# Optimization experiments

Hardware: AMD Instinct MI355X
Metric: run time of the kernel (lower is better)

Reference implementation:

```python
import jax, jax.numpy as jnp
import numpy as np

N_HEADS = 16
D_HEAD = 64
N_ROTATE = 32
ROPE_BASE = 10000.0
MAX_LEN = 2048  # round_up_to_multiple_of_256(keep count); static for jit
BATCH, SEQ = 2, 4096


def setup_inputs() -> dict:
    key = jax.random.key(0)
    kq, kk, kv = jax.random.split(key, 3)
    q = jax.random.normal(kq, (BATCH, N_HEADS, MAX_LEN, D_HEAD), jnp.float32)
    k = jax.random.normal(kk, (BATCH, N_HEADS, SEQ, D_HEAD), jnp.float32)
    v = jax.random.normal(kv, (BATCH, N_HEADS, SEQ, D_HEAD), jnp.float32)
    # causal full mask [batch, seq, seq] and full position ids [batch, seq]
    mask_full = jnp.broadcast_to(jnp.tril(jnp.ones((SEQ, SEQ), bool)), (BATCH, SEQ, SEQ))
    pos_full = jnp.broadcast_to(jnp.arange(SEQ, dtype=jnp.int32), (BATCH, SEQ))
    # skip_mask: exactly MAX_LEN kept tokens per row (random positions)
    rng = np.random.default_rng(0)
    sm = np.zeros((BATCH, SEQ), dtype=bool)
    for i in range(BATCH):
        sm[i, rng.permutation(SEQ)[:MAX_LEN]] = True
    return {"q": q, "k": k, "v": v, "mask_full": mask_full,
            "pos_full": pos_full, "skip_mask": jnp.asarray(sm)}


def _rope_rotate(x, pos):
    # x: [b, h, L, n_rotate], pos: [b, L]
    half = N_ROTATE // 2
    inv_freq = 1.0 / (ROPE_BASE ** (jnp.arange(0, N_ROTATE, 2, dtype=jnp.float32) / N_ROTATE))
    freqs = pos.astype(jnp.float32)[..., None] * inv_freq          # [b, L, half]
    emb = jnp.concatenate([freqs, freqs], axis=-1)[:, None]        # [b, 1, L, n_rotate]
    cos, sin = jnp.cos(emb), jnp.sin(emb)
    x1, x2 = x[..., :half], x[..., half:]
    rot = jnp.concatenate([-x2, x1], axis=-1)                      # rotate_half
    return x * cos + rot * sin


def reference(q, k, v, mask_full, pos_full, skip_mask):
    b, S = skip_mask.shape
    lengths = skip_mask.sum(axis=1)
    # vectorized _trim_attention_mask: stable argsort compacts kept indices to the front
    order = jnp.argsort(jnp.where(skip_mask, 0, 1), axis=1, stable=True)
    idx = order[:, :MAX_LEN]                                       # [b, max_len]
    brow = jnp.arange(b)[:, None]
    mask_trim = mask_full[brow, idx]                               # [b, max_len, S]
    pos_trim = pos_full[brow, idx]                                 # [b, max_len]
    valid = jnp.arange(MAX_LEN)[None, :] < lengths[:, None]
    mask_trim = mask_trim & valid[..., None]
    pos_trim = jnp.where(valid, pos_trim, 0)

    # partial RoPE on first n_rotate channels
    rq = _rope_rotate(q[..., :N_ROTATE], pos_trim)
    rk = _rope_rotate(k[..., :N_ROTATE], pos_full)
    q = jnp.concatenate([rq, q[..., N_ROTATE:]], axis=-1)
    k = jnp.concatenate([rk, k[..., N_ROTATE:]], axis=-1)

    # masked SDPA (bool mask broadcast over heads)
    scale = 1.0 / jnp.sqrt(jnp.float32(D_HEAD))
    scores = jnp.einsum('bhqd,bhkd->bhqk', q, k) * scale
    scores = jnp.where(mask_trim[:, None], scores, jnp.finfo(scores.dtype).min)
    attn = jax.nn.softmax(scores, axis=-1)
    return jnp.einsum('bhqk,bhkd->bhqd', attn, v)
```

## Files before the change

### kernel.cpp

```cpp
#include <hip/hip_runtime.h>
#include <math.h>

#define BB 2
#define HH 16
#define QQ 2048
#define SS 4096
#define DD 64
#define NRH 16
#define NQT 32
#define PBPAD 68

typedef unsigned short u16;
typedef unsigned int   u32;
typedef short bhalf8 __attribute__((ext_vector_type(8)));
typedef float f32x4  __attribute__((ext_vector_type(4)));

typedef __attribute__((address_space(1))) const u32 gu32;
typedef __attribute__((address_space(3))) u32 lu32;

#if __has_builtin(__builtin_amdgcn_exp2f)
#define EXP2(x) __builtin_amdgcn_exp2f(x)
#else
#define EXP2(x) exp2f(x)
#endif

union Frag16 { uint4 u; bhalf8 v; u16 s[8]; uint2 d[2]; };

__device__ __forceinline__ u16 f2bf(float f) {
  union { float f; u32 u; } c; c.f = f;
  return (u16)((c.u + 0x7FFFu + ((c.u >> 16) & 1u)) >> 16);
}

__device__ __forceinline__ bhalf8 ldfrag(const u16* p) {
  Frag16 f; f.u = *reinterpret_cast<const uint4*>(p); return f.v;
}

__device__ __forceinline__ void rope32(float* x, int pos) {
  const float step = 0.8304820237218405f;
  const float fp = (float)pos;
#pragma unroll
  for (int i = 0; i < NRH; ++i) {
    float ang = fp * exp2f(-step * (float)i);
    float sv, cv;
    __sincosf(ang, &sv, &cv);
    float a = x[i], b = x[i + NRH];
    x[i]       = a * cv - b * sv;
    x[i + NRH] = b * cv + a * sv;
  }
}

__global__ void prep_idx_kernel(const unsigned char* __restrict__ sm,
                                int* __restrict__ idx) {
  __shared__ int wsum[4];
  __shared__ int modes;
  const int tid = threadIdx.x;
  const int b = (int)blockIdx.x;

  int c = 0;
  for (int i = 0; i < 32; ++i) c += (sm[tid * 32 + i] != 0) ? 1 : 0;
#pragma unroll
  for (int off = 32; off; off >>= 1) c += __shfl_down(c, off);
  if ((tid & 63) == 0) wsum[tid >> 6] = c;
  __syncthreads();
  if (tid == 0) modes = (wsum[0] + wsum[1] + wsum[2] + wsum[3] > 3000) ? 1 : 0;
  __syncthreads();
  const bool byteMode = (modes != 0);
  const u32* sm32 = (const u32*)sm;

  const int base = b * SS + tid * 16;
  u32 flags = 0;
  for (int i = 0; i < 16; ++i) {
    bool f = byteMode ? (sm[base + i] != 0) : (sm32[base + i] != 0);
    flags |= ((u32)(f ? 1 : 0)) << i;
  }
  int cnt = __popc(flags);
  int vv = cnt;
#pragma unroll
  for (int off = 1; off < 64; off <<= 1) {
    int t = __shfl_up(vv, off);
    if ((tid & 63) >= off) vv += t;
  }
  __syncthreads();
  if ((tid & 63) == 63) wsum[tid >> 6] = vv;
  __syncthreads();
  int add = 0;
  for (int w2 = 0; w2 < (tid >> 6); ++w2) add += wsum[w2];
  int p = vv - cnt + add;
  for (int i = 0; i < 16; ++i) {
    if (flags & (1u << i)) {
      if (p < QQ) idx[b * QQ + p] = tid * 16 + i;
      ++p;
    }
  }
}

__global__ __launch_bounds__(256) void prep_kv_kernel(const float* __restrict__ k,
                                                      const float* __restrict__ v,
                                                      u16* __restrict__ kbf,
                                                      u16* __restrict__ vt) {
  __shared__ u16 tile[64][72];
  if (blockIdx.x < 512) {
    int r = blockIdx.x * 256 + threadIdx.x;
    int pos = r & (SS - 1);
    float x[64];
    const float4* src = (const float4*)(k + (size_t)r * DD);
#pragma unroll
    for (int i = 0; i < 16; ++i) {
      float4 t = src[i];
      x[4 * i] = t.x; x[4 * i + 1] = t.y; x[4 * i + 2] = t.z; x[4 * i + 3] = t.w;
    }
    rope32(x, pos);
    u16 tmp[64];
#pragma unroll
    for (int i = 0; i < 64; ++i) tmp[i] = f2bf(x[i]);
    uint4* dst = (uint4*)(kbf + (size_t)r * DD);
#pragma unroll
    for (int i = 0; i < 8; ++i) dst[i] = ((uint4*)tmp)[i];
  } else {
    int blk = (int)blockIdx.x - 512;
    int bh = blk >> 6;
    int jt = blk & 63;
    int t = threadIdx.x;
    int jl = t >> 2;
    int dc = (t & 3) * 16;
    const float4* src = (const float4*)(v + ((size_t)(bh * SS + jt * 64 + jl)) * DD + dc);
#pragma unroll
    for (int i = 0; i < 4; ++i) {
      float4 f = src[i];
      tile[jl][dc + 4 * i]     = f2bf(f.x);
      tile[jl][dc + 4 * i + 1] = f2bf(f.y);
      tile[jl][dc + 4 * i + 2] = f2bf(f.z);
      tile[jl][dc + 4 * i + 3] = f2bf(f.w);
    }
    __syncthreads();
    int d = t >> 2;
    int js = (t & 3) * 16;
    u16 o[16];
#pragma unroll
    for (int i = 0; i < 16; ++i) o[i] = tile[js + i][d];
    uint4* dst = (uint4*)(vt + ((size_t)(bh * DD + d)) * SS + jt * 64 + js);
    dst[0] = ((uint4*)o)[0];
    dst[1] = ((uint4*)o)[1];
  }
}

__device__ __forceinline__ void stage_tiles(const char* kb_bh, const char* vt_bh,
                                            u16* Kb, u16* Vb, int t0,
                                            int w, int srow, int schk) {
#pragma unroll
  for (int p2 = 0; p2 < 2; ++p2) {
    const int rr = w * 16 + p2 * 8 + srow;
    {
      const char* g = kb_bh + (size_t)(t0 + rr) * 128 + ((schk ^ (rr & 7)) * 16);
      lu32* l = (lu32*)((char*)Kb + (w * 16 + p2 * 8) * 128);
      __builtin_amdgcn_global_load_lds((gu32*)g, l, 16, 0, 0);
    }
    {
      const char* g = vt_bh + (size_t)rr * (SS * 2) + t0 * 2 + ((schk ^ (rr & 7)) * 16);
      lu32* l = (lu32*)((char*)Vb + (w * 16 + p2 * 8) * 128);
      __builtin_amdgcn_global_load_lds((gu32*)g, l, 16, 0, 0);
    }
  }
}

__device__ __forceinline__ void attn_tile(
    const u16* __restrict__ Kb, const u16* __restrict__ Vb, u16* __restrict__ pb,
    int t0, int grp, int col,
    int bnd0, int bnd1, int bnd2, int bnd3,
    bhalf8 qa0, bhalf8 qa1,
    f32x4& acc0, f32x4& acc1, f32x4& acc2, f32x4& acc3,
    float& l0, float& l1, float& l2, float& l3) {
  const int swz = col & 7;
  f32x4 s0 = {0.f, 0.f, 0.f, 0.f}, s1 = s0, s2 = s0, s3 = s0;
  {
    const u16* kr0 = Kb + (0 * 16 + col) * 64;
    const u16* kr1 = Kb + (1 * 16 + col) * 64;
    const u16* kr2 = Kb + (2 * 16 + col) * 64;
    const u16* kr3 = Kb + (3 * 16 + col) * 64;
    s0 = __builtin_amdgcn_mfma_f32_16x16x32_bf16(qa0, ldfrag(kr0 + ((grp ^ swz) * 8)), s0, 0, 0, 0);
    s1 = __builtin_amdgcn_mfma_f32_16x16x32_bf16(qa0, ldfrag(kr1 + ((grp ^ swz) * 8)), s1, 0, 0, 0);
    s2 = __builtin_amdgcn_mfma_f32_16x16x32_bf16(qa0, ldfrag(kr2 + ((grp ^ swz) * 8)), s2, 0, 0, 0);
    s3 = __builtin_amdgcn_mfma_f32_16x16x32_bf16(qa0, ldfrag(kr3 + ((grp ^ swz) * 8)), s3, 0, 0, 0);
    s0 = __builtin_amdgcn_mfma_f32_16x16x32_bf16(qa1, ldfrag(kr0 + (((4 + grp) ^ swz) * 8)), s0, 0, 0, 0);
    s1 = __builtin_amdgcn_mfma_f32_16x16x32_bf16(qa1, ldfrag(kr1 + (((4 + grp) ^ swz) * 8)), s1, 0, 0, 0);
    s2 = __builtin_amdgcn_mfma_f32_16x16x32_bf16(qa1, ldfrag(kr2 + (((4 + grp) ^ swz) * 8)), s2, 0, 0, 0);
    s3 = __builtin_amdgcn_mfma_f32_16x16x32_bf16(qa1, ldfrag(kr3 + (((4 + grp) ^ swz) * 8)), s3, 0, 0, 0);
  }

  const int key0 = t0 + col, key1 = t0 + 16 + col, key2 = t0 + 32 + col, key3 = t0 + 48 + col;
#define SM_ROW(R, BND, LACC)                                                   \
  {                                                                            \
    float p0 = (key0 <= (BND)) ? EXP2(s0[R] - 16.f) : 0.f;                     \
    float p1 = (key1 <= (BND)) ? EXP2(s1[R] - 16.f) : 0.f;                     \
    float p2v = (key2 <= (BND)) ? EXP2(s2[R] - 16.f) : 0.f;                    \
    float p3 = (key3 <= (BND)) ? EXP2(s3[R] - 16.f) : 0.f;                     \
    (LACC) += (p0 + p1) + (p2v + p3);                                          \
    u16* prow = pb + (grp * 4 + (R)) * PBPAD;                                  \
    prow[col] = f2bf(p0); prow[16 + col] = f2bf(p1);                           \
    prow[32 + col] = f2bf(p2v); prow[48 + col] = f2bf(p3);                     \
  }
  SM_ROW(0, bnd0, l0)
  SM_ROW(1, bnd1, l1)
  SM_ROW(2, bnd2, l2)
  SM_ROW(3, bnd3, l3)
#undef SM_ROW

  bhalf8 pa0, pa1;
  {
    const u16* p = pb + col * PBPAD;
    Frag16 f0, f1;
    f0.d[0] = *(const uint2*)(p + grp * 8);
    f0.d[1] = *(const uint2*)(p + grp * 8 + 4);
    f1.d[0] = *(const uint2*)(p + 32 + grp * 8);
    f1.d[1] = *(const uint2*)(p + 32 + grp * 8 + 4);
    pa0 = f0.v; pa1 = f1.v;
  }

  {
    const u16* vr0 = Vb + (0 * 16 + col) * 64;
    const u16* vr1 = Vb + (1 * 16 + col) * 64;
    const u16* vr2 = Vb + (2 * 16 + col) * 64;
    const u16* vr3 = Vb + (3 * 16 + col) * 64;
    acc0 = __builtin_amdgcn_mfma_f32_16x16x32_bf16(pa0, ldfrag(vr0 + ((grp ^ swz) * 8)), acc0, 0, 0, 0);
    acc1 = __builtin_amdgcn_mfma_f32_16x16x32_bf16(pa0, ldfrag(vr1 + ((grp ^ swz) * 8)), acc1, 0, 0, 0);
    acc2 = __builtin_amdgcn_mfma_f32_16x16x32_bf16(pa0, ldfrag(vr2 + ((grp ^ swz) * 8)), acc2, 0, 0, 0);
    acc3 = __builtin_amdgcn_mfma_f32_16x16x32_bf16(pa0, ldfrag(vr3 + ((grp ^ swz) * 8)), acc3, 0, 0, 0);
    acc0 = __builtin_amdgcn_mfma_f32_16x16x32_bf16(pa1, ldfrag(vr0 + (((4 + grp) ^ swz) * 8)), acc0, 0, 0, 0);
    acc1 = __builtin_amdgcn_mfma_f32_16x16x32_bf16(pa1, ldfrag(vr1 + (((4 + grp) ^ swz) * 8)), acc1, 0, 0, 0);
    acc2 = __builtin_amdgcn_mfma_f32_16x16x32_bf16(pa1, ldfrag(vr2 + (((4 + grp) ^ swz) * 8)), acc2, 0, 0, 0);
    acc3 = __builtin_amdgcn_mfma_f32_16x16x32_bf16(pa1, ldfrag(vr3 + (((4 + grp) ^ swz) * 8)), acc3, 0, 0, 0);
  }
}

__global__ __launch_bounds__(256) void attn_mfma_kernel(
    const float* __restrict__ qsrc, const u16* __restrict__ kbf,
    const u16* __restrict__ vt, const int* __restrict__ idx,
    float* __restrict__ out) {
  __shared__ u16 KbufA[64 * 64];
  __shared__ u16 VbufA[64 * 64];
  __shared__ u16 KbufB[64 * 64];
  __shared__ u16 VbufB[64 * 64];
  __shared__ u16 Pbuf[4][16 * PBPAD];

  const int blk = (int)blockIdx.x;
  const int bh  = blk & 31;
  const int pr  = blk >> 5;
  const int b   = bh >> 4;
  const int tid  = threadIdx.x;
  const int w    = tid >> 6;
  const int lane = tid & 63;
  const int grp  = lane >> 4;
  const int col  = lane & 15;

  const char* kb_bh = (const char*)(kbf + (size_t)bh * SS * DD);
  const char* vt_bh = (const char*)(vt + (size_t)bh * DD * SS);

  const int srow = lane >> 3;
  const int schk = lane & 7;

  u16* pb = Pbuf[w];

  for (int pass = 0; pass < 2; ++pass) {
    const int qt = pass ? (NQT - 1 - pr) : pr;
    const int q0 = qt * 64;

    const int bnd0 = idx[b * QQ + q0 + w * 16 + grp * 4 + 0];
    const int bnd1 = idx[b * QQ + q0 + w * 16 + grp * 4 + 1];
    const int bnd2 = idx[b * QQ + q0 + w * 16 + grp * 4 + 2];
    const int bnd3 = idx[b * QQ + q0 + w * 16 + grp * 4 + 3];
    const int maxbound = idx[b * QQ + q0 + 63];
    const int ntiles = (maxbound >> 6) + 1;

    bhalf8 qa0, qa1;
    {
      const int qrow = q0 + w * 16 + col;
      const int mypos = idx[b * QQ + qrow];
      const float* qr = qsrc + (size_t)(bh * QQ + qrow) * DD;
      const int lof = (grp & 1) * 8;
      float4 A0 = *(const float4*)(qr + lof);
      float4 A1 = *(const float4*)(qr + lof + 4);
      float4 B0 = *(const float4*)(qr + 16 + lof);
      float4 B1 = *(const float4*)(qr + 16 + lof + 4);
      float4 C0 = *(const float4*)(qr + 32 + grp * 8);
      float4 C1 = *(const float4*)(qr + 32 + grp * 8 + 4);
      float xlo[8] = {A0.x, A0.y, A0.z, A0.w, A1.x, A1.y, A1.z, A1.w};
      float xhi[8] = {B0.x, B0.y, B0.z, B0.w, B1.x, B1.y, B1.z, B1.w};
      float xq1[8] = {C0.x, C0.y, C0.z, C0.w, C1.x, C1.y, C1.z, C1.w};
      const float scq = 0.125f * 1.44269504088896f;
      const float fp = (float)mypos;
      Frag16 f0, f1;
#pragma unroll
      for (int j = 0; j < 8; ++j) {
        float ang = fp * exp2f(-0.8304820237218405f * (float)(lof + j));
        float sv, cv;
        __sincosf(ang, &sv, &cv);
        float val = (grp >= 2) ? (xhi[j] * cv + xlo[j] * sv)
                               : (xlo[j] * cv - xhi[j] * sv);
        f0.s[j] = f2bf(val * scq);
        f1.s[j] = f2bf(xq1[j] * scq);
      }
      qa0 = f0.v; qa1 = f1.v;
    }

    f32x4 acc0 = {0.f, 0.f, 0.f, 0.f}, acc1 = acc0, acc2 = acc0, acc3 = acc0;
    float l0 = 0.f, l1 = 0.f, l2 = 0.f, l3 = 0.f;

    stage_tiles(kb_bh, vt_bh, KbufA, VbufA, 0, w, srow, schk);
    __syncthreads();

    for (int ti = 0; ti < ntiles; ti += 2) {
      const bool has1 = (ti + 1) < ntiles;
      if (has1) stage_tiles(kb_bh, vt_bh, KbufB, VbufB, (ti + 1) << 6, w, srow, schk);
      attn_tile(KbufA, VbufA, pb, ti << 6, grp, col, bnd0, bnd1, bnd2, bnd3,
                qa0, qa1, acc0, acc1, acc2, acc3, l0, l1, l2, l3);
      __syncthreads();
      if (has1) {
        if (ti + 2 < ntiles)
          stage_tiles(kb_bh, vt_bh, KbufA, VbufA, (ti + 2) << 6, w, srow, schk);
        attn_tile(KbufB, VbufB, pb, (ti + 1) << 6, grp, col, bnd0, bnd1, bnd2, bnd3,
                  qa0, qa1, acc0, acc1, acc2, acc3, l0, l1, l2, l3);
        __syncthreads();
      }
    }

#pragma unroll
    for (int mdel = 1; mdel < 16; mdel <<= 1) {
      l0 += __shfl_xor(l0, mdel);
      l1 += __shfl_xor(l1, mdel);
      l2 += __shfl_xor(l2, mdel);
      l3 += __shfl_xor(l3, mdel);
    }
    float i0 = 1.f / l0, i1 = 1.f / l1, i2 = 1.f / l2, i3 = 1.f / l3;
    float* ob = out + (size_t)(bh * QQ + q0 + w * 16 + grp * 4) * DD + col;
#pragma unroll
    for (int r = 0; r < 4; ++r) {
      float iv = (r == 0) ? i0 : (r == 1) ? i1 : (r == 2) ? i2 : i3;
      ob[(size_t)r * DD + 0]  = acc0[r] * iv;
      ob[(size_t)r * DD + 16] = acc1[r] * iv;
      ob[(size_t)r * DD + 32] = acc2[r] * iv;
      ob[(size_t)r * DD + 48] = acc3[r] * iv;
    }
  }
}

__global__ __launch_bounds__(64) void attn_fb_kernel(const float* __restrict__ q,
                                                     const float* __restrict__ ksrc,
                                                     const float* __restrict__ v,
                                                     const int* __restrict__ idx,
                                                     float* __restrict__ out) {
  int t = (int)(gridDim.x - 1u - blockIdx.x);
  int sub = t >> 5;
  int bh = t & 31;
  int b = bh >> 4;
  int lane = threadIdx.x;
  int qi = sub * 64 + lane;
  const int bound = idx[b * QQ + qi];

  float qreg[64];
  {
    const float4* qp = (const float4*)(q + ((size_t)bh * QQ + qi) * DD);
#pragma unroll
    for (int i = 0; i < 16; ++i) {
      float4 t4 = qp[i];
      qreg[4 * i] = t4.x; qreg[4 * i + 1] = t4.y;
      qreg[4 * i + 2] = t4.z; qreg[4 * i + 3] = t4.w;
    }
  }
  rope32(qreg, bound);
#pragma unroll
  for (int i = 0; i < 64; ++i) qreg[i] *= 0.125f;

  const float* kbase = ksrc + (size_t)bh * SS * DD;
  const float* vbase = v + (size_t)bh * SS * DD;
  float acc[64];
#pragma unroll
  for (int i = 0; i < 64; ++i) acc[i] = 0.f;
  float mrun = -INFINITY, lrun = 0.f;

  for (int j = 0; j <= bound; ++j) {
    float ka[64];
    const float4* kp = (const float4*)(kbase + (size_t)j * DD);
#pragma unroll
    for (int i = 0; i < 16; ++i) {
      float4 t4 = kp[i];
      ka[4 * i] = t4.x; ka[4 * i + 1] = t4.y;
      ka[4 * i + 2] = t4.z; ka[4 * i + 3] = t4.w;
    }
    rope32(ka, j);
    float s0 = 0.f, s1 = 0.f, s2 = 0.f, s3 = 0.f;
#pragma unroll
    for (int i = 0; i < 16; ++i) {
      s0 = fmaf(qreg[4 * i], ka[4 * i], s0);
      s1 = fmaf(qreg[4 * i + 1], ka[4 * i + 1], s1);
      s2 = fmaf(qreg[4 * i + 2], ka[4 * i + 2], s2);
      s3 = fmaf(qreg[4 * i + 3], ka[4 * i + 3], s3);
    }
    float sc = (s0 + s1) + (s2 + s3);
    if (sc > mrun) {
      float alpha = __expf(mrun - sc);
      lrun *= alpha;
#pragma unroll
      for (int i = 0; i < 64; ++i) acc[i] *= alpha;
      mrun = sc;
    }
    float pw = __expf(sc - mrun);
    lrun += pw;
    const float4* vp = (const float4*)(vbase + (size_t)j * DD);
#pragma unroll
    for (int i = 0; i < 16; ++i) {
      float4 t4 = vp[i];
      acc[4 * i] = fmaf(pw, t4.x, acc[4 * i]);
      acc[4 * i + 1] = fmaf(pw, t4.y, acc[4 * i + 1]);
      acc[4 * i + 2] = fmaf(pw, t4.z, acc[4 * i + 2]);
      acc[4 * i + 3] = fmaf(pw, t4.w, acc[4 * i + 3]);
    }
  }
  float inv = 1.0f / lrun;
  float4* op = (float4*)(out + ((size_t)bh * QQ + qi) * DD);
#pragma unroll
  for (int i = 0; i < 16; ++i) {
    float4 t4;
    t4.x = acc[4 * i] * inv; t4.y = acc[4 * i + 1] * inv;
    t4.z = acc[4 * i + 2] * inv; t4.w = acc[4 * i + 3] * inv;
    op[i] = t4;
  }
}

extern "C" void kernel_launch(void* const* d_in, const int* in_sizes, int n_in,
                              void* d_out, int out_size, void* d_ws, size_t ws_size,
                              hipStream_t stream) {
  (void)in_sizes; (void)n_in; (void)out_size;
  const float* q = (const float*)d_in[0];
  const float* k = (const float*)d_in[1];
  const float* v = (const float*)d_in[2];
  const unsigned char* skip = (const unsigned char*)d_in[5];
  float* out = (float*)d_out;

  char* base = (char*)d_ws;
  int* idx = (int*)base;
  const size_t kbytes = (size_t)BB * HH * SS * DD * 2;
  u16* kbf = (u16*)(base + 16384);
  u16* vtb = (u16*)(base + 16384 + kbytes);
  const size_t need = 16384 + 2 * kbytes;

  prep_idx_kernel<<<2, 256, 0, stream>>>(skip, idx);
  if (ws_size >= need) {
    prep_kv_kernel<<<512 + BB * HH * 64, 256, 0, stream>>>(k, v, kbf, vtb);
    attn_mfma_kernel<<<(NQT / 2) * 32, 256, 0, stream>>>(q, kbf, vtb, idx, out);
  } else {
    attn_fb_kernel<<<1024, 64, 0, stream>>>(q, k, v, idx, out);
  }
}
```

Baseline: 317.9 us.

## Fuse prep and attention into one cooperative kernel with grid sync

Merges the index-compaction, K RoPE/bf16 conversion, V transpose and attention kernels into a single cooperative launch of 512 blocks, separated by a grid-wide barrier, so two kernel launches and their gaps go away. The QK MFMA operands are swapped so each lane owns one query row's scores. This enables a wave-uniform fast path that skips per-element masking when the whole tile is below the wave's minimum bound, and lets P be written as packed bf16 pairs. The risks are the cost of the grid sync, occupancy limits from cooperative launch with the launch bound of 2 blocks per CU, and less parallelism in the prep phase.

```diff
diff --git a/kernel.cpp b/kernel.cpp
--- a/kernel.cpp
+++ b/kernel.cpp
@@ -1,4 +1,6 @@
 #include <hip/hip_runtime.h>
+#include <hip/hip_cooperative_groups.h>
+#include <hip/hip_bf16.h>
 #include <math.h>
 
 #define BB 2
@@ -31,6 +33,11 @@
   return (u16)((c.u + 0x7FFFu + ((c.u >> 16) & 1u)) >> 16);
 }
 
+__device__ __forceinline__ u32 pk2(float a, float b) {
+  __hip_bfloat162 h = __float22bfloat162_rn(make_float2(a, b));
+  union { __hip_bfloat162 h; u32 u; } c; c.h = h; return c.u;
+}
+
 __device__ __forceinline__ bhalf8 ldfrag(const u16* p) {
   Frag16 f; f.u = *reinterpret_cast<const uint4*>(p); return f.v;
 }
@@ -49,101 +56,6 @@
   }
 }
 
-__global__ void prep_idx_kernel(const unsigned char* __restrict__ sm,
-                                int* __restrict__ idx) {
-  __shared__ int wsum[4];
-  __shared__ int modes;
-  const int tid = threadIdx.x;
-  const int b = (int)blockIdx.x;
-
-  int c = 0;
-  for (int i = 0; i < 32; ++i) c += (sm[tid * 32 + i] != 0) ? 1 : 0;
-#pragma unroll
-  for (int off = 32; off; off >>= 1) c += __shfl_down(c, off);
-  if ((tid & 63) == 0) wsum[tid >> 6] = c;
-  __syncthreads();
-  if (tid == 0) modes = (wsum[0] + wsum[1] + wsum[2] + wsum[3] > 3000) ? 1 : 0;
-  __syncthreads();
-  const bool byteMode = (modes != 0);
-  const u32* sm32 = (const u32*)sm;
-
-  const int base = b * SS + tid * 16;
-  u32 flags = 0;
-  for (int i = 0; i < 16; ++i) {
-    bool f = byteMode ? (sm[base + i] != 0) : (sm32[base + i] != 0);
-    flags |= ((u32)(f ? 1 : 0)) << i;
-  }
-  int cnt = __popc(flags);
-  int vv = cnt;
-#pragma unroll
-  for (int off = 1; off < 64; off <<= 1) {
-    int t = __shfl_up(vv, off);
-    if ((tid & 63) >= off) vv += t;
-  }
-  __syncthreads();
-  if ((tid & 63) == 63) wsum[tid >> 6] = vv;
-  __syncthreads();
-  int add = 0;
-  for (int w2 = 0; w2 < (tid >> 6); ++w2) add += wsum[w2];
-  int p = vv - cnt + add;
-  for (int i = 0; i < 16; ++i) {
-    if (flags & (1u << i)) {
-      if (p < QQ) idx[b * QQ + p] = tid * 16 + i;
-      ++p;
-    }
-  }
-}
-
-__global__ __launch_bounds__(256) void prep_kv_kernel(const float* __restrict__ k,
-                                                      const float* __restrict__ v,
-                                                      u16* __restrict__ kbf,
-                                                      u16* __restrict__ vt) {
-  __shared__ u16 tile[64][72];
-  if (blockIdx.x < 512) {
-    int r = blockIdx.x * 256 + threadIdx.x;
-    int pos = r & (SS - 1);
-    float x[64];
-    const float4* src = (const float4*)(k + (size_t)r * DD);
-#pragma unroll
-    for (int i = 0; i < 16; ++i) {
-      float4 t = src[i];
-      x[4 * i] = t.x; x[4 * i + 1] = t.y; x[4 * i + 2] = t.z; x[4 * i + 3] = t.w;
-    }
-    rope32(x, pos);
-    u16 tmp[64];
-#pragma unroll
-    for (int i = 0; i < 64; ++i) tmp[i] = f2bf(x[i]);
-    uint4* dst = (uint4*)(kbf + (size_t)r * DD);
-#pragma unroll
-    for (int i = 0; i < 8; ++i) dst[i] = ((uint4*)tmp)[i];
-  } else {
-    int blk = (int)blockIdx.x - 512;
-    int bh = blk >> 6;
-    int jt = blk & 63;
-    int t = threadIdx.x;
-    int jl = t >> 2;
-    int dc = (t & 3) * 16;
-    const float4* src = (const float4*)(v + ((size_t)(bh * SS + jt * 64 + jl)) * DD + dc);
-#pragma unroll
-    for (int i = 0; i < 4; ++i) {
-      float4 f = src[i];
-      tile[jl][dc + 4 * i]     = f2bf(f.x);
-      tile[jl][dc + 4 * i + 1] = f2bf(f.y);
-      tile[jl][dc + 4 * i + 2] = f2bf(f.z);
-      tile[jl][dc + 4 * i + 3] = f2bf(f.w);
-    }
-    __syncthreads();
-    int d = t >> 2;
-    int js = (t & 3) * 16;
-    u16 o[16];
-#pragma unroll
-    for (int i = 0; i < 16; ++i) o[i] = tile[js + i][d];
-    uint4* dst = (uint4*)(vt + ((size_t)(bh * DD + d)) * SS + jt * 64 + js);
-    dst[0] = ((uint4*)o)[0];
-    dst[1] = ((uint4*)o)[1];
-  }
-}
-
 __device__ __forceinline__ void stage_tiles(const char* kb_bh, const char* vt_bh,
                                             u16* Kb, u16* Vb, int t0,
                                             int w, int srow, int schk) {
@@ -165,11 +77,9 @@
 
 __device__ __forceinline__ void attn_tile(
     const u16* __restrict__ Kb, const u16* __restrict__ Vb, u16* __restrict__ pb,
-    int t0, int grp, int col,
-    int bnd0, int bnd1, int bnd2, int bnd3,
+    int t0, int grp, int col, int bnd, int bmin,
     bhalf8 qa0, bhalf8 qa1,
-    f32x4& acc0, f32x4& acc1, f32x4& acc2, f32x4& acc3,
-    float& l0, float& l1, float& l2, float& l3) {
+    f32x4& acc0, f32x4& acc1, f32x4& acc2, f32x4& acc3, float& l) {
   const int swz = col & 7;
   f32x4 s0 = {0.f, 0.f, 0.f, 0.f}, s1 = s0, s2 = s0, s3 = s0;
   {
@@ -177,33 +87,56 @@
     const u16* kr1 = Kb + (1 * 16 + col) * 64;
     const u16* kr2 = Kb + (2 * 16 + col) * 64;
     const u16* kr3 = Kb + (3 * 16 + col) * 64;
-    s0 = __builtin_amdgcn_mfma_f32_16x16x32_bf16(qa0, ldfrag(kr0 + ((grp ^ swz) * 8)), s0, 0, 0, 0);
-    s1 = __builtin_amdgcn_mfma_f32_16x16x32_bf16(qa0, ldfrag(kr1 + ((grp ^ swz) * 8)), s1, 0, 0, 0);
-    s2 = __builtin_amdgcn_mfma_f32_16x16x32_bf16(qa0, ldfrag(kr2 + ((grp ^ swz) * 8)), s2, 0, 0, 0);
-    s3 = __builtin_amdgcn_mfma_f32_16x16x32_bf16(qa0, ldfrag(kr3 + ((grp ^ swz) * 8)), s3, 0, 0, 0);
-    s0 = __builtin_amdgcn_mfma_f32_16x16x32_bf16(qa1, ldfrag(kr0 + (((4 + grp) ^ swz) * 8)), s0, 0, 0, 0);
-    s1 = __builtin_amdgcn_mfma_f32_16x16x32_bf16(qa1, ldfrag(kr1 + (((4 + grp) ^ swz) * 8)), s1, 0, 0, 0);
-    s2 = __builtin_amdgcn_mfma_f32_16x16x32_bf16(qa1, ldfrag(kr2 + (((4 + grp) ^ swz) * 8)), s2, 0, 0, 0);
-    s3 = __builtin_amdgcn_mfma_f32_16x16x32_bf16(qa1, ldfrag(kr3 + (((4 + grp) ^ swz) * 8)), s3, 0, 0, 0);
-  }
-
-  const int key0 = t0 + col, key1 = t0 + 16 + col, key2 = t0 + 32 + col, key3 = t0 + 48 + col;
-#define SM_ROW(R, BND, LACC)                                                   \
-  {                                                                            \
-    float p0 = (key0 <= (BND)) ? EXP2(s0[R] - 16.f) : 0.f;                     \
-    float p1 = (key1 <= (BND)) ? EXP2(s1[R] - 16.f) : 0.f;                     \
-    float p2v = (key2 <= (BND)) ? EXP2(s2[R] - 16.f) : 0.f;                    \
-    float p3 = (key3 <= (BND)) ? EXP2(s3[R] - 16.f) : 0.f;                     \
-    (LACC) += (p0 + p1) + (p2v + p3);                                          \
-    u16* prow = pb + (grp * 4 + (R)) * PBPAD;                                  \
-    prow[col] = f2bf(p0); prow[16 + col] = f2bf(p1);                           \
-    prow[32 + col] = f2bf(p2v); prow[48 + col] = f2bf(p3);                     \
-  }
-  SM_ROW(0, bnd0, l0)
-  SM_ROW(1, bnd1, l1)
-  SM_ROW(2, bnd2, l2)
-  SM_ROW(3, bnd3, l3)
-#undef SM_ROW
+    s0 = __builtin_amdgcn_mfma_f32_16x16x32_bf16(ldfrag(kr0 + ((grp ^ swz) * 8)), qa0, s0, 0, 0, 0);
+    s1 = __builtin_amdgcn_mfma_f32_16x16x32_bf16(ldfrag(kr1 + ((grp ^ swz) * 8)), qa0, s1, 0, 0, 0);
+    s2 = __builtin_amdgcn_mfma_f32_16x16x32_bf16(ldfrag(kr2 + ((grp ^ swz) * 8)), qa0, s2, 0, 0, 0);
+    s3 = __builtin_amdgcn_mfma_f32_16x16x32_bf16(ldfrag(kr3 + ((grp ^ swz) * 8)), qa0, s3, 0, 0, 0);
+    s0 = __builtin_amdgcn_mfma_f32_16x16x32_bf16(ldfrag(kr0 + (((4 + grp) ^ swz) * 8)), qa1, s0, 0, 0, 0);
+    s1 = __builtin_amdgcn_mfma_f32_16x16x32_bf16(ldfrag(kr1 + (((4 + grp) ^ swz) * 8)), qa1, s1, 0, 0, 0);
+    s2 = __builtin_amdgcn_mfma_f32_16x16x32_bf16(ldfrag(kr2 + (((4 + grp) ^ swz) * 8)), qa1, s2, 0, 0, 0);
+    s3 = __builtin_amdgcn_mfma_f32_16x16x32_bf16(ldfrag(kr3 + (((4 + grp) ^ swz) * 8)), qa1, s3, 0, 0, 0);
+  }
+
+  float pv0, pv1, pv2, pv3, pv4, pv5, pv6, pv7;
+  float pv8, pv9, pvA, pvB, pvC, pvD, pvE, pvF;
+  if (t0 + 63 <= bmin) {
+    pv0 = EXP2(s0[0] - 16.f); pv1 = EXP2(s0[1] - 16.f);
+    pv2 = EXP2(s0[2] - 16.f); pv3 = EXP2(s0[3] - 16.f);
+    pv4 = EXP2(s1[0] - 16.f); pv5 = EXP2(s1[1] - 16.f);
+    pv6 = EXP2(s1[2] - 16.f); pv7 = EXP2(s1[3] - 16.f);
+    pv8 = EXP2(s2[0] - 16.f); pv9 = EXP2(s2[1] - 16.f);
+    pvA = EXP2(s2[2] - 16.f); pvB = EXP2(s2[3] - 16.f);
+    pvC = EXP2(s3[0] - 16.f); pvD = EXP2(s3[1] - 16.f);
+    pvE = EXP2(s3[2] - 16.f); pvF = EXP2(s3[3] - 16.f);
+  } else {
+    const int cc = bnd - t0 - grp * 4;
+    pv0 = (0  <= cc) ? EXP2(s0[0] - 16.f) : 0.f;
+    pv1 = (1  <= cc) ? EXP2(s0[1] - 16.f) : 0.f;
+    pv2 = (2  <= cc) ? EXP2(s0[2] - 16.f) : 0.f;
+    pv3 = (3  <= cc) ? EXP2(s0[3] - 16.f) : 0.f;
+    pv4 = (16 <= cc) ? EXP2(s1[0] - 16.f) : 0.f;
+    pv5 = (17 <= cc) ? EXP2(s1[1] - 16.f) : 0.f;
+    pv6 = (18 <= cc) ? EXP2(s1[2] - 16.f) : 0.f;
+    pv7 = (19 <= cc) ? EXP2(s1[3] - 16.f) : 0.f;
+    pv8 = (32 <= cc) ? EXP2(s2[0] - 16.f) : 0.f;
+    pv9 = (33 <= cc) ? EXP2(s2[1] - 16.f) : 0.f;
+    pvA = (34 <= cc) ? EXP2(s2[2] - 16.f) : 0.f;
+    pvB = (35 <= cc) ? EXP2(s2[3] - 16.f) : 0.f;
+    pvC = (48 <= cc) ? EXP2(s3[0] - 16.f) : 0.f;
+    pvD = (49 <= cc) ? EXP2(s3[1] - 16.f) : 0.f;
+    pvE = (50 <= cc) ? EXP2(s3[2] - 16.f) : 0.f;
+    pvF = (51 <= cc) ? EXP2(s3[3] - 16.f) : 0.f;
+  }
+  l += (((pv0 + pv1) + (pv2 + pv3)) + ((pv4 + pv5) + (pv6 + pv7))) +
+       (((pv8 + pv9) + (pvA + pvB)) + ((pvC + pvD) + (pvE + pvF)));
+
+  {
+    u16* base = pb + col * PBPAD + grp * 4;
+    *(uint2*)(base + 0)  = make_uint2(pk2(pv0, pv1), pk2(pv2, pv3));
+    *(uint2*)(base + 16) = make_uint2(pk2(pv4, pv5), pk2(pv6, pv7));
+    *(uint2*)(base + 32) = make_uint2(pk2(pv8, pv9), pk2(pvA, pvB));
+    *(uint2*)(base + 48) = make_uint2(pk2(pvC, pvD), pk2(pvE, pvF));
+  }
 
   bhalf8 pa0, pa1;
   {
@@ -232,21 +165,114 @@
   }
 }
 
-__global__ __launch_bounds__(256) void attn_mfma_kernel(
-    const float* __restrict__ qsrc, const u16* __restrict__ kbf,
-    const u16* __restrict__ vt, const int* __restrict__ idx,
+__global__ __launch_bounds__(256, 2) void fused_kernel(
+    const float* __restrict__ q, const float* __restrict__ k,
+    const float* __restrict__ v, const unsigned char* __restrict__ skip,
+    u16* __restrict__ kbf, u16* __restrict__ vt, int* __restrict__ idx,
     float* __restrict__ out) {
-  __shared__ u16 KbufA[64 * 64];
-  __shared__ u16 VbufA[64 * 64];
-  __shared__ u16 KbufB[64 * 64];
-  __shared__ u16 VbufB[64 * 64];
-  __shared__ u16 Pbuf[4][16 * PBPAD];
+  __shared__ __align__(16) char SMEM[41472];
+  __shared__ int wsum[4];
+  __shared__ int modes;
 
   const int blk = (int)blockIdx.x;
+  const int tid = threadIdx.x;
+
+  {
+    int r = blk * 256 + tid;
+    int pos = r & (SS - 1);
+    float x[64];
+    const float4* src = (const float4*)(k + (size_t)r * DD);
+#pragma unroll
+    for (int i = 0; i < 16; ++i) {
+      float4 t = src[i];
+      x[4 * i] = t.x; x[4 * i + 1] = t.y; x[4 * i + 2] = t.z; x[4 * i + 3] = t.w;
+    }
+    rope32(x, pos);
+    u16 tmp[64];
+#pragma unroll
+    for (int i = 0; i < 64; ++i) tmp[i] = f2bf(x[i]);
+    uint4* dst = (uint4*)(kbf + (size_t)r * DD);
+#pragma unroll
+    for (int i = 0; i < 8; ++i) dst[i] = ((uint4*)tmp)[i];
+  }
+
+  {
+    u16* tile = (u16*)SMEM;
+    const int jl = tid >> 2, dc = (tid & 3) * 16;
+    const int d = tid >> 2, js = (tid & 3) * 16;
+#pragma unroll 1
+    for (int it = 0; it < 4; ++it) {
+      int tl = blk * 4 + it;
+      int bh = tl >> 6, jt = tl & 63;
+      const float4* src = (const float4*)(v + ((size_t)(bh * SS + jt * 64 + jl)) * DD + dc);
+      float4 f0 = src[0], f1 = src[1], f2 = src[2], f3 = src[3];
+      __syncthreads();
+      u16* tr = tile + jl * 72 + dc;
+      tr[0]  = f2bf(f0.x); tr[1]  = f2bf(f0.y); tr[2]  = f2bf(f0.z); tr[3]  = f2bf(f0.w);
+      tr[4]  = f2bf(f1.x); tr[5]  = f2bf(f1.y); tr[6]  = f2bf(f1.z); tr[7]  = f2bf(f1.w);
+      tr[8]  = f2bf(f2.x); tr[9]  = f2bf(f2.y); tr[10] = f2bf(f2.z); tr[11] = f2bf(f2.w);
+      tr[12] = f2bf(f3.x); tr[13] = f2bf(f3.y); tr[14] = f2bf(f3.z); tr[15] = f2bf(f3.w);
+      __syncthreads();
+      u16 o[16];
+#pragma unroll
+      for (int i = 0; i < 16; ++i) o[i] = tile[(js + i) * 72 + d];
+      uint4* dst = (uint4*)(vt + ((size_t)(bh * DD + d)) * SS + jt * 64 + js);
+      dst[0] = ((uint4*)o)[0];
+      dst[1] = ((uint4*)o)[1];
+    }
+  }
+
+  if (blk < BB) {
+    const int b = blk;
+    int c = 0;
+    for (int i = 0; i < 32; ++i) c += (skip[tid * 32 + i] != 0) ? 1 : 0;
+#pragma unroll
+    for (int off = 32; off; off >>= 1) c += __shfl_down(c, off);
+    __syncthreads();
+    if ((tid & 63) == 0) wsum[tid >> 6] = c;
+    __syncthreads();
+    if (tid == 0) modes = (wsum[0] + wsum[1] + wsum[2] + wsum[3] > 3000) ? 1 : 0;
+    __syncthreads();
+    const bool byteMode = (modes != 0);
+    const u32* sm32 = (const u32*)skip;
+    const int base = b * SS + tid * 16;
+    u32 flags = 0;
+    for (int i = 0; i < 16; ++i) {
+      bool f = byteMode ? (skip[base + i] != 0) : (sm32[base + i] != 0);
+      flags |= ((u32)(f ? 1 : 0)) << i;
+    }
+    int cnt = __popc(flags);
+    int vv = cnt;
+#pragma unroll
+    for (int off = 1; off < 64; off <<= 1) {
+      int t = __shfl_up(vv, off);
+      if ((tid & 63) >= off) vv += t;
+    }
+    __syncthreads();
+    if ((tid & 63) == 63) wsum[tid >> 6] = vv;
+    __syncthreads();
+    int add = 0;
+    for (int w2 = 0; w2 < (tid >> 6); ++w2) add += wsum[w2];
+    int p = vv - cnt + add;
+    for (int i = 0; i < 16; ++i) {
+      if (flags & (1u << i)) {
+        if (p < QQ) idx[b * QQ + p] = tid * 16 + i;
+        ++p;
+      }
+    }
+  }
+
+  cooperative_groups::this_grid().sync();
+
+  u16* KA = (u16*)SMEM;
+  u16* VA = KA + 4096;
+  u16* KB = VA + 4096;
+  u16* VB = KB + 4096;
+  u16* pball = (u16*)(SMEM + 32768);
+
   const int bh  = blk & 31;
   const int pr  = blk >> 5;
   const int b   = bh >> 4;
-  const int tid  = threadIdx.x;
   const int w    = tid >> 6;
   const int lane = tid & 63;
   const int grp  = lane >> 4;
@@ -254,28 +280,22 @@
 
   const char* kb_bh = (const char*)(kbf + (size_t)bh * SS * DD);
   const char* vt_bh = (const char*)(vt + (size_t)bh * DD * SS);
-
   const int srow = lane >> 3;
   const int schk = lane & 7;
-
-  u16* pb = Pbuf[w];
+  u16* pb = pball + w * 16 * PBPAD;
 
   for (int pass = 0; pass < 2; ++pass) {
     const int qt = pass ? (NQT - 1 - pr) : pr;
     const int q0 = qt * 64;
 
-    const int bnd0 = idx[b * QQ + q0 + w * 16 + grp * 4 + 0];
-    const int bnd1 = idx[b * QQ + q0 + w * 16 + grp * 4 + 1];
-    const int bnd2 = idx[b * QQ + q0 + w * 16 + grp * 4 + 2];
-    const int bnd3 = idx[b * QQ + q0 + w * 16 + grp * 4 + 3];
+    const int bnd = idx[b * QQ + q0 + w * 16 + col];
+    const int bmin = __builtin_amdgcn_readfirstlane(bnd);
     const int maxbound = idx[b * QQ + q0 + 63];
     const int ntiles = (maxbound >> 6) + 1;
 
     bhalf8 qa0, qa1;
     {
-      const int qrow = q0 + w * 16 + col;
-      const int mypos = idx[b * QQ + qrow];
-      const float* qr = qsrc + (size_t)(bh * QQ + qrow) * DD;
+      const float* qr = q + (size_t)(bh * QQ + q0 + w * 16 + col) * DD;
       const int lof = (grp & 1) * 8;
       float4 A0 = *(const float4*)(qr + lof);
       float4 A1 = *(const float4*)(qr + lof + 4);
@@ -287,7 +307,7 @@
       float xhi[8] = {B0.x, B0.y, B0.z, B0.w, B1.x, B1.y, B1.z, B1.w};
       float xq1[8] = {C0.x, C0.y, C0.z, C0.w, C1.x, C1.y, C1.z, C1.w};
       const float scq = 0.125f * 1.44269504088896f;
-      const float fp = (float)mypos;
+      const float fp = (float)bnd;
       Frag16 f0, f1;
 #pragma unroll
       for (int j = 0; j < 8; ++j) {
@@ -303,42 +323,82 @@
     }
 
     f32x4 acc0 = {0.f, 0.f, 0.f, 0.f}, acc1 = acc0, acc2 = acc0, acc3 = acc0;
-    float l0 = 0.f, l1 = 0.f, l2 = 0.f, l3 = 0.f;
-
-    stage_tiles(kb_bh, vt_bh, KbufA, VbufA, 0, w, srow, schk);
+    float l = 0.f;
+
+    stage_tiles(kb_bh, vt_bh, KA, VA, 0, w, srow, schk);
     __syncthreads();
 
     for (int ti = 0; ti < ntiles; ti += 2) {
       const bool has1 = (ti + 1) < ntiles;
-      if (has1) stage_tiles(kb_bh, vt_bh, KbufB, VbufB, (ti + 1) << 6, w, srow, schk);
-      attn_tile(KbufA, VbufA, pb, ti << 6, grp, col, bnd0, bnd1, bnd2, bnd3,
-                qa0, qa1, acc0, acc1, acc2, acc3, l0, l1, l2, l3);
+      if (has1) stage_tiles(kb_bh, vt_bh, KB, VB, (ti + 1) << 6, w, srow, schk);
+      attn_tile(KA, VA, pb, ti << 6, grp, col, bnd, bmin, qa0, qa1,
+                acc0, acc1, acc2, acc3, l);
       __syncthreads();
       if (has1) {
         if (ti + 2 < ntiles)
-          stage_tiles(kb_bh, vt_bh, KbufA, VbufA, (ti + 2) << 6, w, srow, schk);
-        attn_tile(KbufB, VbufB, pb, (ti + 1) << 6, grp, col, bnd0, bnd1, bnd2, bnd3,
-                  qa0, qa1, acc0, acc1, acc2, acc3, l0, l1, l2, l3);
+          stage_tiles(kb_bh, vt_bh, KA, VA, (ti + 2) << 6, w, srow, schk);
+        attn_tile(KB, VB, pb, (ti + 1) << 6, grp, col, bnd, bmin, qa0, qa1,
+                  acc0, acc1, acc2, acc3, l);
         __syncthreads();
       }
     }
 
-#pragma unroll
-    for (int mdel = 1; mdel < 16; mdel <<= 1) {
-      l0 += __shfl_xor(l0, mdel);
-      l1 += __shfl_xor(l1, mdel);
-      l2 += __shfl_xor(l2, mdel);
-      l3 += __shfl_xor(l3, mdel);
-    }
-    float i0 = 1.f / l0, i1 = 1.f / l1, i2 = 1.f / l2, i3 = 1.f / l3;
+    l += __shfl_xor(l, 16);
+    l += __shfl_xor(l, 32);
     float* ob = out + (size_t)(bh * QQ + q0 + w * 16 + grp * 4) * DD + col;
 #pragma unroll
     for (int r = 0; r < 4; ++r) {
-      float iv = (r == 0) ? i0 : (r == 1) ? i1 : (r == 2) ? i2 : i3;
+      float lr = __shfl(l, grp * 4 + r);
+      float iv = 1.f / lr;
       ob[(size_t)r * DD + 0]  = acc0[r] * iv;
       ob[(size_t)r * DD + 16] = acc1[r] * iv;
       ob[(size_t)r * DD + 32] = acc2[r] * iv;
       ob[(size_t)r * DD + 48] = acc3[r] * iv;
+    }
+  }
+}
+
+__global__ void prep_idx_kernel(const unsigned char* __restrict__ sm,
+                                int* __restrict__ idx) {
+  __shared__ int wsum[4];
+  __shared__ int modes;
+  const int tid = threadIdx.x;
+  const int b = (int)blockIdx.x;
+
+  int c = 0;
+  for (int i = 0; i < 32; ++i) c += (sm[tid * 32 + i] != 0) ? 1 : 0;
+#pragma unroll
+  for (int off = 32; off; off >>= 1) c += __shfl_down(c, off);
+  if ((tid & 63) == 0) wsum[tid >> 6] = c;
+  __syncthreads();
+  if (tid == 0) modes = (wsum[0] + wsum[1] + wsum[2] + wsum[3] > 3000) ? 1 : 0;
+  __syncthreads();
+  const bool byteMode = (modes != 0);
+  const u32* sm32 = (const u32*)sm;
+
+  const int base = b * SS + tid * 16;
+  u32 flags = 0;
+  for (int i = 0; i < 16; ++i) {
+    bool f = byteMode ? (sm[base + i] != 0) : (sm32[base + i] != 0);
+    flags |= ((u32)(f ? 1 : 0)) << i;
+  }
+  int cnt = __popc(flags);
+  int vv = cnt;
+#pragma unroll
+  for (int off = 1; off < 64; off <<= 1) {
+    int t = __shfl_up(vv, off);
+    if ((tid & 63) >= off) vv += t;
+  }
+  __syncthreads();
+  if ((tid & 63) == 63) wsum[tid >> 6] = vv;
+  __syncthreads();
+  int add = 0;
+  for (int w2 = 0; w2 < (tid >> 6); ++w2) add += wsum[w2];
+  int p = vv - cnt + add;
+  for (int i = 0; i < 16; ++i) {
+    if (flags & (1u << i)) {
+      if (p < QQ) idx[b * QQ + p] = tid * 16 + i;
+      ++p;
     }
   }
 }
@@ -443,11 +503,13 @@
   u16* vtb = (u16*)(base + 16384 + kbytes);
   const size_t need = 16384 + 2 * kbytes;
 
-  prep_idx_kernel<<<2, 256, 0, stream>>>(skip, idx);
   if (ws_size >= need) {
-    prep_kv_kernel<<<512 + BB * HH * 64, 256, 0, stream>>>(k, v, kbf, vtb);
-    attn_mfma_kernel<<<(NQT / 2) * 32, 256, 0, stream>>>(q, kbf, vtb, idx, out);
+    void* args[] = {(void*)&q, (void*)&k, (void*)&v, (void*)&skip,
+                    (void*)&kbf, (void*)&vtb, (void*)&idx, (void*)&out};
+    hipLaunchCooperativeKernel((void*)fused_kernel, dim3(512), dim3(256),
+                               args, 0, stream);
   } else {
+    prep_idx_kernel<<<2, 256, 0, stream>>>(skip, idx);
     attn_fb_kernel<<<1024, 64, 0, stream>>>(q, k, v, idx, out);
   }
 }
```

Measured after the change: 394.2 us. 24.0% more time.
